# Kernel optimization log

Measured on AMD Instinct MI355X. Metric: run time of the kernel, lower is better.

The kernel has to match this reference:

```python
import jax, jax.numpy as jnp
import numpy as np

BS, SL, H, DH = 2, 2048, 32, 128
STRIDE = 16
NUM_PAGES = BS * (SL // STRIDE)  # 256, distinct page per block
PAGE_DIM = 1 * 2 * STRIDE * H * DH  # blocks * partitions * stride * kv_heads * head_dim


def setup_inputs() -> dict:
    key = jax.random.key(0)
    k1, k2, k3 = jax.random.split(key, 3)
    xq = jax.random.normal(k1, (BS, SL, H, DH), dtype=jnp.float32)
    xk = jax.random.normal(k2, (BS, SL, H, DH), dtype=jnp.float32)
    xv = jax.random.normal(k3, (BS, SL, H, DH), dtype=jnp.float32)
    cache_state = jnp.zeros((NUM_PAGES, PAGE_DIM), dtype=jnp.float32)
    seq_block_ids = jnp.arange(BS * (SL // STRIDE), dtype=jnp.int64 if jax.config.jax_enable_x64 else jnp.int32).reshape(BS, SL // STRIDE)
    return {"xq": xq, "xk": xk, "xv": xv, "cache_state": cache_state, "seq_block_ids": seq_block_ids}


def reference(xq, xk, xv, cache_state, seq_block_ids):
    bs, sl, h, dh = xq.shape
    nb = sl // STRIDE  # blocks per sequence
    num_pages = cache_state.shape[0]

    # --- paged cache write (prefill path: start_positions is None) ---
    # page layout: [page, transformer_block(=1), partition(k=0,v=1), stride, head, head_dim]
    cache = cache_state.reshape(num_pages, 1, 2, STRIDE, h, dh)
    pids = seq_block_ids.reshape(-1)  # [bs*nb]
    k_blocks = xk.reshape(bs * nb, STRIDE, h, dh)
    v_blocks = xv.reshape(bs * nb, STRIDE, h, dh)
    cache = cache.at[pids, 0, 0].set(k_blocks)
    cache = cache.at[pids, 0, 1].set(v_blocks)
    new_cache_state = cache.reshape(cache_state.shape)

    # --- GQA repeat_kv: n_rep = head_count // head_count_kv = 1 -> no-op ---

    # --- SDPA, attn_mask=None, is_causal=False ---
    scale = 1.0 / np.sqrt(dh).astype(np.float32)
    scores = jnp.einsum("bqhd,bkhd->bhqk", xq, xk) * scale  # [bs, h, sl, sl]
    attn = jax.nn.softmax(scores, axis=-1)
    out = jnp.einsum("bhqk,bkhd->bqhd", attn, xv)
    attn_output = out.reshape(bs, sl, h * dh)
    return attn_output, new_cache_state
```

## Files before the change

### kernel.cpp

```cpp
#include <hip/hip_runtime.h>
#include <hip/hip_bf16.h>
#include <stdint.h>

#define BS 2
#define SL 2048
#define H 32
#define DH 128
#define ATT_ELEMS (BS*SL*H*DH)
#define KTILES (SL/64)
#define KT32 (SL/32)
#define QSCALE (0.08838834764831845f * 1.4426950408889634f)
#define MFIX 10.0f

typedef __attribute__((ext_vector_type(8))) short short8_t;
typedef __attribute__((ext_vector_type(16))) float f32x16_t;
typedef __attribute__((ext_vector_type(4))) unsigned int u32x4_t;
typedef __attribute__((ext_vector_type(2))) unsigned int u32x2_t;

union FragU { u32x4_t u; short8_t s; };

__device__ __forceinline__ unsigned short f2bf(float x){
    union { float f; unsigned int u; } v; v.f = x;
    unsigned int r = v.u + 0x7fffu + ((v.u >> 16) & 1u);
    return (unsigned short)(r >> 16);
}
__device__ __forceinline__ unsigned int pack2(float a, float b){
    return (unsigned int)f2bf(a) | ((unsigned int)f2bf(b) << 16);
}
__device__ __forceinline__ unsigned int cvtpk(float a, float b){
    unsigned int r;
    asm("v_cvt_pk_bf16_f32 %0, %1, %2" : "=v"(r) : "v"(a), "v"(b));
    return r;
}
__device__ __forceinline__ void gload16(const unsigned short* g, unsigned short* l){
    __builtin_amdgcn_global_load_lds(
        (const __attribute__((address_space(1))) void*)(const void*)g,
        (__attribute__((address_space(3))) void*)(void*)l, 16, 0, 0);
}

__global__ __launch_bounds__(256) void prep_kv_kernel(const float* __restrict__ xk,
                                                      const float* __restrict__ xv,
                                                      const int* __restrict__ pids,
                                                      unsigned short* __restrict__ kfr,
                                                      unsigned short* __restrict__ vfr,
                                                      float* __restrict__ out_cache,
                                                      int do_cache){
    __shared__ unsigned short tK[64*136];
    __shared__ unsigned short tV[64*136];
    int tile = blockIdx.x, h = blockIdx.y, b = blockIdx.z;
    int tid = threadIdx.x;
    size_t tb = ((size_t)((b*H + h)*KTILES + tile)) * 8192;
    int pg[4];
    #pragma unroll
    for (int j = 0; j < 4; ++j) pg[j] = pids[b*128 + tile*4 + j];

    #pragma unroll
    for (int i = 0; i < 8; ++i){
        int c = tid + 256*i;
        int row = c >> 5, f4 = c & 31;
        size_t gidx = ((size_t)((b*SL + tile*64 + row)*H + h))*DH + f4*4;
        float4 kx = *(const float4*)(xk + gidx);
        float4 vx = *(const float4*)(xv + gidx);
        u32x2_t kw; kw[0] = pack2(kx.x, kx.y); kw[1] = pack2(kx.z, kx.w);
        u32x2_t vw; vw[0] = pack2(vx.x, vx.y); vw[1] = pack2(vx.z, vx.w);
        *(u32x2_t*)(&tK[row*136 + f4*4]) = kw;
        *(u32x2_t*)(&tV[row*136 + f4*4]) = vw;
        if (do_cache){
            size_t cb = (size_t)pg[row>>4]*131072 + (size_t)(row&15)*4096 + h*128 + f4*4;
            *(float4*)(out_cache + cb)         = kx;
            *(float4*)(out_cache + cb + 65536) = vx;
        }
    }
    __syncthreads();
    #pragma unroll
    for (int i = 0; i < 4; ++i){
        int c = tid + 256*i;
        int sub = c >> 9, c2 = c & 511;
        int fi = c2 >> 6, l = c2 & 63;
        int key = sub*32 + (l & 31);
        int d0  = fi*16 + (l >> 5)*8;
        u32x4_t w = *(const u32x4_t*)(&tK[key*136 + d0]);
        *(u32x4_t*)(&kfr[tb + (size_t)sub*4096 + (size_t)c2*8]) = w;
    }
    #pragma unroll
    for (int i = 0; i < 4; ++i){
        int c = tid + 256*i;
        int sub = c >> 9, c2 = c & 511;
        int fi = c2 >> 6, l = c2 & 63;
        int d  = (fi >> 1)*32 + (l & 31);
        int k0 = sub*32 + (fi & 1)*16 + (l >> 5)*8;
        u32x4_t u;
        #pragma unroll
        for (int w = 0; w < 4; ++w)
            u[w] = (unsigned)tV[(k0+2*w)*136 + d] | ((unsigned)tV[(k0+2*w+1)*136 + d] << 16);
        *(u32x4_t*)(&vfr[tb + (size_t)sub*4096 + (size_t)c2*8]) = u;
    }
}

__global__ __launch_bounds__(256) void cache_scatter_kernel(const float* __restrict__ xk,
                                                            const float* __restrict__ xv,
                                                            const int* __restrict__ pids,
                                                            float* __restrict__ out_cache){
    int sb = blockIdx.x >> 1, part = blockIdx.x & 1;
    int page = pids[sb];
    const float4* s4 = (const float4*)((part ? xv : xk) + (size_t)sb * 65536);
    float4* d4 = (float4*)(out_cache + (size_t)page * 131072 + (size_t)part * 65536);
    int base = blockIdx.y * 2048 + threadIdx.x;
    #pragma unroll
    for (int i = 0; i < 8; ++i) d4[base + i*256] = s4[base + i*256];
}

__global__ __launch_bounds__(256, 4) void attn_kernel(const float* __restrict__ xq,
                                                      const unsigned short* __restrict__ kfr,
                                                      const unsigned short* __restrict__ vfr,
                                                      float* __restrict__ out){
    __shared__ unsigned short smem[2*8192];

    const int tid  = threadIdx.x;
    const int lane = tid & 63;
    const int wave = tid >> 6;
    const int l31  = lane & 31;
    const int hi   = lane >> 5;

    int lin = blockIdx.x;
    int swz = (lin & 7)*128 + (lin >> 3);
    const int qblk = swz & 15;
    const int h    = (swz >> 4) & 31;
    const int b    = swz >> 9;
    const int qbase = qblk*128 + wave*32;

    short8_t qf[8];
    {
        const float* qptr = xq + ((size_t)((b*SL + qbase + l31)*H + h))*DH + hi*8;
        #pragma unroll
        for (int f = 0; f < 8; ++f){
            float4 a = *(const float4*)(qptr + f*16);
            float4 c = *(const float4*)(qptr + f*16 + 4);
            FragU w;
            w.u[0] = pack2(a.x*QSCALE, a.y*QSCALE);
            w.u[1] = pack2(a.z*QSCALE, a.w*QSCALE);
            w.u[2] = pack2(c.x*QSCALE, c.y*QSCALE);
            w.u[3] = pack2(c.z*QSCALE, c.w*QSCALE);
            qf[f] = w.s;
        }
    }

    f32x16_t acc[4];
    #pragma unroll
    for (int d = 0; d < 4; ++d)
        #pragma unroll
        for (int r = 0; r < 16; ++r) acc[d][r] = 0.f;
    float l_run = 0.f;

    const size_t bh = (size_t)(b*H + h) * ((size_t)KT32*4096);
    const unsigned short* kg = kfr + bh;
    const unsigned short* vg = vfr + bh;

    #pragma unroll
    for (int i = 0; i < 2; ++i){
        int ch = wave*2 + i;
        gload16(kg + ch*512 + lane*8, smem + ch*512);
        gload16(vg + ch*512 + lane*8, smem + 4096 + ch*512);
    }
    asm volatile("s_waitcnt vmcnt(0)" ::: "memory");
    __builtin_amdgcn_s_barrier();
    asm volatile("" ::: "memory");

    #pragma unroll 1
    for (int t = 0; t < KT32; ++t){
        const int p = t & 1;
        const unsigned short* Kc = smem + p*8192;
        const unsigned short* Vc = Kc + 4096;

        if (t + 1 < KT32){
            const unsigned short* kn = kg + (size_t)(t+1)*4096;
            const unsigned short* vn = vg + (size_t)(t+1)*4096;
            unsigned short* Kn = smem + (p^1)*8192;
            #pragma unroll
            for (int i = 0; i < 2; ++i){
                int ch = wave*2 + i;
                gload16(kn + ch*512 + lane*8, Kn + ch*512);
                gload16(vn + ch*512 + lane*8, Kn + 4096 + ch*512);
            }
        }
        __builtin_amdgcn_sched_barrier(0);

        f32x16_t s;
        #pragma unroll
        for (int r = 0; r < 16; ++r) s[r] = -MFIX;
        __builtin_amdgcn_s_setprio(1);
        #pragma unroll
        for (int f = 0; f < 8; ++f){
            FragU kf; kf.u = *(const u32x4_t*)(&Kc[f*512 + lane*8]);
            s = __builtin_amdgcn_mfma_f32_32x32x16_bf16(kf.s, qf[f], s, 0, 0, 0);
        }
        __builtin_amdgcn_s_setprio(0);

        float lsum = 0.f;
        FragU pf[2];
        #define PSLICE(KS, RB)                                                              \
        {                                                                                   \
            float e0 = __builtin_amdgcn_exp2f(s[RB+0]);                                     \
            float e1 = __builtin_amdgcn_exp2f(s[RB+1]);                                     \
            float e2 = __builtin_amdgcn_exp2f(s[RB+2]);                                     \
            float e3 = __builtin_amdgcn_exp2f(s[RB+3]);                                     \
            float e4 = __builtin_amdgcn_exp2f(s[RB+4]);                                     \
            float e5 = __builtin_amdgcn_exp2f(s[RB+5]);                                     \
            float e6 = __builtin_amdgcn_exp2f(s[RB+6]);                                     \
            float e7 = __builtin_amdgcn_exp2f(s[RB+7]);                                     \
            lsum += ((e0+e1)+(e2+e3)) + ((e4+e5)+(e6+e7));                                  \
            unsigned a  = cvtpk(e0,e1), bq = cvtpk(e2,e3);                                  \
            unsigned cq = cvtpk(e4,e5), dq = cvtpk(e6,e7);                                  \
            unsigned y0 = hi ? a : cq,  y1 = hi ? bq : dq;                                  \
            unsigned r0 = __shfl_xor(y0, 32, 64);                                           \
            unsigned r1 = __shfl_xor(y1, 32, 64);                                           \
            pf[KS].u[0] = hi ? r0 : a;  pf[KS].u[1] = hi ? r1 : bq;                         \
            pf[KS].u[2] = hi ? cq : r0; pf[KS].u[3] = hi ? dq : r1;                         \
        }
        PSLICE(0, 0)
        PSLICE(1, 8)
        #undef PSLICE
        lsum += __shfl_xor(lsum, 32, 64);
        l_run += lsum;

        __builtin_amdgcn_s_setprio(1);
        #pragma unroll
        for (int dblk = 0; dblk < 4; ++dblk){
            #pragma unroll
            for (int ks = 0; ks < 2; ++ks){
                FragU vb;
                vb.u = *(const u32x4_t*)(&Vc[(dblk*2 + ks)*512 + lane*8]);
                acc[dblk] = __builtin_amdgcn_mfma_f32_32x32x16_bf16(pf[ks].s, vb.s, acc[dblk], 0, 0, 0);
            }
        }
        __builtin_amdgcn_s_setprio(0);

        if (t + 1 < KT32){
            asm volatile("s_waitcnt vmcnt(0)" ::: "memory");
            __builtin_amdgcn_s_barrier();
            asm volatile("" ::: "memory");
        }
    }

    float linv = 1.f / l_run;
    float lr[16];
    #pragma unroll
    for (int r = 0; r < 16; ++r)
        lr[r] = __shfl(linv, (r&3) + 8*(r>>2) + 4*hi, 64);
    #pragma unroll
    for (int dblk = 0; dblk < 4; ++dblk){
        #pragma unroll
        for (int r = 0; r < 16; ++r){
            int q = qbase + (r&3) + 8*(r>>2) + 4*hi;
            out[(size_t)(b*SL + q)*(H*DH) + h*DH + dblk*32 + l31] = acc[dblk][r] * lr[r];
        }
    }
}

extern "C" void kernel_launch(void* const* d_in, const int* in_sizes, int n_in,
                              void* d_out, int out_size, void* d_ws, size_t ws_size,
                              hipStream_t stream) {
    const float* xq = (const float*)d_in[0];
    const float* xk = (const float*)d_in[1];
    const float* xv = (const float*)d_in[2];
    const int* pids = (const int*)d_in[4];

    float* out_attn  = (float*)d_out;
    float* out_cache = out_attn + (size_t)ATT_ELEMS;

    const size_t frag_elems = (size_t)BS*H*KTILES*8192;
    const size_t need       = 2*frag_elems*sizeof(unsigned short);

    if (ws_size >= need){
        unsigned short* kfr = (unsigned short*)d_ws;
        unsigned short* vfr = kfr + frag_elems;
        prep_kv_kernel<<<dim3(KTILES, H, BS), 256, 0, stream>>>(xk, xv, pids, kfr, vfr, out_cache, 1);
        attn_kernel<<<dim3(BS*H*(SL/128)), 256, 0, stream>>>(xq, kfr, vfr, out_attn);
    } else {
        unsigned short* vfr = (unsigned short*)out_cache;
        unsigned short* kfr = vfr + frag_elems;
        prep_kv_kernel<<<dim3(KTILES, H, BS), 256, 0, stream>>>(xk, xv, pids, kfr, vfr, out_cache, 0);
        attn_kernel<<<dim3(BS*H*(SL/128)), 256, 0, stream>>>(xq, kfr, vfr, out_attn);
        cache_scatter_kernel<<<dim3(512, 8), 256, 0, stream>>>(xk, xv, pids, out_cache);
    }
}
```

Measured before the change: 219.7 us.

## Process two 32-row query tiles per wave to reuse K/V fragments

```diff
diff --git a/kernel.cpp b/kernel.cpp
--- a/kernel.cpp
+++ b/kernel.cpp
@@ -110,7 +110,7 @@
     for (int i = 0; i < 8; ++i) d4[base + i*256] = s4[base + i*256];
 }
 
-__global__ __launch_bounds__(256, 4) void attn_kernel(const float* __restrict__ xq,
+__global__ __launch_bounds__(256, 2) void attn_kernel(const float* __restrict__ xq,
                                                       const unsigned short* __restrict__ kfr,
                                                       const unsigned short* __restrict__ vfr,
                                                       float* __restrict__ out){
@@ -123,15 +123,16 @@
     const int hi   = lane >> 5;
 
     int lin = blockIdx.x;
-    int swz = (lin & 7)*128 + (lin >> 3);
-    const int qblk = swz & 15;
-    const int h    = (swz >> 4) & 31;
-    const int b    = swz >> 9;
-    const int qbase = qblk*128 + wave*32;
-
-    short8_t qf[8];
-    {
-        const float* qptr = xq + ((size_t)((b*SL + qbase + l31)*H + h))*DH + hi*8;
+    int swz = (lin & 7)*64 + (lin >> 3);
+    const int qblk = swz & 7;
+    const int h    = (swz >> 3) & 31;
+    const int b    = swz >> 8;
+    const int qbase = qblk*256 + wave*64;
+
+    short8_t qf0[8], qf1[8];
+    #pragma unroll
+    for (int qb = 0; qb < 2; ++qb){
+        const float* qptr = xq + ((size_t)((b*SL + qbase + qb*32 + l31)*H + h))*DH + hi*8;
         #pragma unroll
         for (int f = 0; f < 8; ++f){
             float4 a = *(const float4*)(qptr + f*16);
@@ -141,16 +142,16 @@
             w.u[1] = pack2(a.z*QSCALE, a.w*QSCALE);
             w.u[2] = pack2(c.x*QSCALE, c.y*QSCALE);
             w.u[3] = pack2(c.z*QSCALE, c.w*QSCALE);
-            qf[f] = w.s;
-        }
-    }
-
-    f32x16_t acc[4];
+            if (qb == 0) qf0[f] = w.s; else qf1[f] = w.s;
+        }
+    }
+
+    f32x16_t acc0[4], acc1[4];
     #pragma unroll
     for (int d = 0; d < 4; ++d)
         #pragma unroll
-        for (int r = 0; r < 16; ++r) acc[d][r] = 0.f;
-    float l_run = 0.f;
+        for (int r = 0; r < 16; ++r){ acc0[d][r] = 0.f; acc1[d][r] = 0.f; }
+    float l0 = 0.f, l1 = 0.f;
 
     const size_t bh = (size_t)(b*H + h) * ((size_t)KT32*4096);
     const unsigned short* kg = kfr + bh;
@@ -185,43 +186,43 @@
         }
         __builtin_amdgcn_sched_barrier(0);
 
-        f32x16_t s;
-        #pragma unroll
-        for (int r = 0; r < 16; ++r) s[r] = -MFIX;
+        f32x16_t s0, s1;
+        #pragma unroll
+        for (int r = 0; r < 16; ++r){ s0[r] = -MFIX; s1[r] = -MFIX; }
         __builtin_amdgcn_s_setprio(1);
         #pragma unroll
         for (int f = 0; f < 8; ++f){
             FragU kf; kf.u = *(const u32x4_t*)(&Kc[f*512 + lane*8]);
-            s = __builtin_amdgcn_mfma_f32_32x32x16_bf16(kf.s, qf[f], s, 0, 0, 0);
+            s0 = __builtin_amdgcn_mfma_f32_32x32x16_bf16(kf.s, qf0[f], s0, 0, 0, 0);
+            s1 = __builtin_amdgcn_mfma_f32_32x32x16_bf16(kf.s, qf1[f], s1, 0, 0, 0);
         }
         __builtin_amdgcn_s_setprio(0);
 
-        float lsum = 0.f;
-        FragU pf[2];
-        #define PSLICE(KS, RB)                                                              \
+        FragU pf0[2], pf1[2];
+        #define PSLICE(SV, PF, KS, RB, LR)                                                  \
         {                                                                                   \
-            float e0 = __builtin_amdgcn_exp2f(s[RB+0]);                                     \
-            float e1 = __builtin_amdgcn_exp2f(s[RB+1]);                                     \
-            float e2 = __builtin_amdgcn_exp2f(s[RB+2]);                                     \
-            float e3 = __builtin_amdgcn_exp2f(s[RB+3]);                                     \
-            float e4 = __builtin_amdgcn_exp2f(s[RB+4]);                                     \
-            float e5 = __builtin_amdgcn_exp2f(s[RB+5]);                                     \
-            float e6 = __builtin_amdgcn_exp2f(s[RB+6]);                                     \
-            float e7 = __builtin_amdgcn_exp2f(s[RB+7]);                                     \
-            lsum += ((e0+e1)+(e2+e3)) + ((e4+e5)+(e6+e7));                                  \
+            float e0 = __builtin_amdgcn_exp2f(SV[RB+0]);                                    \
+            float e1 = __builtin_amdgcn_exp2f(SV[RB+1]);                                    \
+            float e2 = __builtin_amdgcn_exp2f(SV[RB+2]);                                    \
+            float e3 = __builtin_amdgcn_exp2f(SV[RB+3]);                                    \
+            float e4 = __builtin_amdgcn_exp2f(SV[RB+4]);                                    \
+            float e5 = __builtin_amdgcn_exp2f(SV[RB+5]);                                    \
+            float e6 = __builtin_amdgcn_exp2f(SV[RB+6]);                                    \
+            float e7 = __builtin_amdgcn_exp2f(SV[RB+7]);                                    \
+            LR += ((e0+e1)+(e2+e3)) + ((e4+e5)+(e6+e7));                                    \
             unsigned a  = cvtpk(e0,e1), bq = cvtpk(e2,e3);                                  \
             unsigned cq = cvtpk(e4,e5), dq = cvtpk(e6,e7);                                  \
             unsigned y0 = hi ? a : cq,  y1 = hi ? bq : dq;                                  \
             unsigned r0 = __shfl_xor(y0, 32, 64);                                           \
             unsigned r1 = __shfl_xor(y1, 32, 64);                                           \
-            pf[KS].u[0] = hi ? r0 : a;  pf[KS].u[1] = hi ? r1 : bq;                         \
-            pf[KS].u[2] = hi ? cq : r0; pf[KS].u[3] = hi ? dq : r1;                         \
-        }
-        PSLICE(0, 0)
-        PSLICE(1, 8)
+            PF[KS].u[0] = hi ? r0 : a;  PF[KS].u[1] = hi ? r1 : bq;                         \
+            PF[KS].u[2] = hi ? cq : r0; PF[KS].u[3] = hi ? dq : r1;                         \
+        }
+        PSLICE(s0, pf0, 0, 0, l0)
+        PSLICE(s0, pf0, 1, 8, l0)
+        PSLICE(s1, pf1, 0, 0, l1)
+        PSLICE(s1, pf1, 1, 8, l1)
         #undef PSLICE
-        lsum += __shfl_xor(lsum, 32, 64);
-        l_run += lsum;
 
         __builtin_amdgcn_s_setprio(1);
         #pragma unroll
@@ -230,7 +231,8 @@
             for (int ks = 0; ks < 2; ++ks){
                 FragU vb;
                 vb.u = *(const u32x4_t*)(&Vc[(dblk*2 + ks)*512 + lane*8]);
-                acc[dblk] = __builtin_amdgcn_mfma_f32_32x32x16_bf16(pf[ks].s, vb.s, acc[dblk], 0, 0, 0);
+                acc0[dblk] = __builtin_amdgcn_mfma_f32_32x32x16_bf16(pf0[ks].s, vb.s, acc0[dblk], 0, 0, 0);
+                acc1[dblk] = __builtin_amdgcn_mfma_f32_32x32x16_bf16(pf1[ks].s, vb.s, acc1[dblk], 0, 0, 0);
             }
         }
         __builtin_amdgcn_s_setprio(0);
@@ -242,17 +244,25 @@
         }
     }
 
-    float linv = 1.f / l_run;
-    float lr[16];
-    #pragma unroll
-    for (int r = 0; r < 16; ++r)
-        lr[r] = __shfl(linv, (r&3) + 8*(r>>2) + 4*hi, 64);
-    #pragma unroll
-    for (int dblk = 0; dblk < 4; ++dblk){
-        #pragma unroll
-        for (int r = 0; r < 16; ++r){
-            int q = qbase + (r&3) + 8*(r>>2) + 4*hi;
-            out[(size_t)(b*SL + q)*(H*DH) + h*DH + dblk*32 + l31] = acc[dblk][r] * lr[r];
+    l0 += __shfl_xor(l0, 32, 64);
+    l1 += __shfl_xor(l1, 32, 64);
+
+    #pragma unroll
+    for (int qb = 0; qb < 2; ++qb){
+        float linv = 1.f / (qb ? l1 : l0);
+        float lr[16];
+        #pragma unroll
+        for (int r = 0; r < 16; ++r)
+            lr[r] = __shfl(linv, (r&3) + 8*(r>>2) + 4*hi, 64);
+        int q0 = qbase + qb*32;
+        #pragma unroll
+        for (int dblk = 0; dblk < 4; ++dblk){
+            #pragma unroll
+            for (int r = 0; r < 16; ++r){
+                int q = q0 + (r&3) + 8*(r>>2) + 4*hi;
+                float v = (qb ? acc1[dblk][r] : acc0[dblk][r]) * lr[r];
+                out[(size_t)(b*SL + q)*(H*DH) + h*DH + dblk*32 + l31] = v;
+            }
         }
     }
 }
@@ -275,12 +285,12 @@
         unsigned short* kfr = (unsigned short*)d_ws;
         unsigned short* vfr = kfr + frag_elems;
         prep_kv_kernel<<<dim3(KTILES, H, BS), 256, 0, stream>>>(xk, xv, pids, kfr, vfr, out_cache, 1);
-        attn_kernel<<<dim3(BS*H*(SL/128)), 256, 0, stream>>>(xq, kfr, vfr, out_attn);
+        attn_kernel<<<dim3(BS*H*(SL/256)), 256, 0, stream>>>(xq, kfr, vfr, out_attn);
     } else {
         unsigned short* vfr = (unsigned short*)out_cache;
         unsigned short* kfr = vfr + frag_elems;
         prep_kv_kernel<<<dim3(KTILES, H, BS), 256, 0, stream>>>(xk, xv, pids, kfr, vfr, out_cache, 0);
-        attn_kernel<<<dim3(BS*H*(SL/128)), 256, 0, stream>>>(xq, kfr, vfr, out_attn);
+        attn_kernel<<<dim3(BS*H*(SL/256)), 256, 0, stream>>>(xq, kfr, vfr, out_attn);
         cache_scatter_kernel<<<dim3(512, 8), 256, 0, stream>>>(xk, xv, pids, out_cache);
     }
 }
```

Result: faster. 214.5 us (-2.4%).
